# Kernel optimization log

Hardware: AMD Instinct MI355X
Metric: run time of the kernel (lower is better)

## Reference

```python
import jax, jax.numpy as jnp
import numpy as np

N = 50000   # nodes
E = 409600  # edges
H = 2       # heads
C = 64      # per-head channels


def _seg_softmax(alpha, dst, n):
    # PyG-style softmax over edges grouped by destination node. alpha: [E, H]
    m = jax.ops.segment_max(alpha, dst, num_segments=n)
    m = jnp.where(jnp.isfinite(m), m, 0.0)
    ex = jnp.exp(alpha - m[dst])
    s = jax.ops.segment_sum(ex, dst, num_segments=n)
    return ex / (s[dst] + 1e-16)


def _tconv(x, src, dst, e, Wq, bq, Wk, bk, Wv, bv, We, Ws, bs, n):
    # PyG TransformerConv (concat=True, beta=False, root_weight=True, dropout=0)
    q = (x @ Wq + bq).reshape(n, H, C)
    k = (x @ Wk + bk).reshape(n, H, C)
    v = (x @ Wv + bv).reshape(n, H, C)
    eh = (e @ We).reshape(-1, H, C)          # lin_edge has no bias in PyG
    kj = k[src] + eh                          # [E, H, C]
    alpha = (q[dst] * kj).sum(-1) / jnp.sqrt(jnp.float32(C))  # [E, H]
    alpha = _seg_softmax(alpha, dst, n)
    msg = (v[src] + eh) * alpha[:, :, None]   # [E, H, C]
    out = jax.ops.segment_sum(msg, dst, num_segments=n).reshape(n, H * C)
    return out + x @ Ws + bs                  # root/skip connection


def setup_inputs() -> dict:
    key = jax.random.key(0)
    ks = jax.random.split(key, 32)

    def lin_w(k, i, o):
        return (jax.random.normal(k, (i, o), dtype=jnp.float32) / np.sqrt(i)).astype(jnp.float32)

    inp = {
        "x": jax.random.normal(ks[0], (N, 6), dtype=jnp.float32),
        "edge_index": jax.random.randint(ks[1], (2, E), 0, N, dtype=jnp.int32).astype(jnp.int64),
        "edge_attr": jax.random.normal(ks[2], (E, 1), dtype=jnp.float32),
        # edge encoder: Linear(1, 64)
        "We_enc": lin_w(ks[3], 1, 64), "be_enc": jnp.zeros((64,), jnp.float32),
        # conv1: TransformerConv(6, 64, heads=2, edge_dim=64)
        "Wq1": lin_w(ks[4], 6, H * C), "bq1": jnp.zeros((H * C,), jnp.float32),
        "Wk1": lin_w(ks[5], 6, H * C), "bk1": jnp.zeros((H * C,), jnp.float32),
        "Wv1": lin_w(ks[6], 6, H * C), "bv1": jnp.zeros((H * C,), jnp.float32),
        "We1": lin_w(ks[7], 64, H * C),
        "Ws1": lin_w(ks[8], 6, H * C), "bs1": jnp.zeros((H * C,), jnp.float32),
        # conv2: TransformerConv(128, 64, heads=2, edge_dim=64)
        "Wq2": lin_w(ks[9], 128, H * C), "bq2": jnp.zeros((H * C,), jnp.float32),
        "Wk2": lin_w(ks[10], 128, H * C), "bk2": jnp.zeros((H * C,), jnp.float32),
        "Wv2": lin_w(ks[11], 128, H * C), "bv2": jnp.zeros((H * C,), jnp.float32),
        "We2": lin_w(ks[12], 64, H * C),
        "Ws2": lin_w(ks[13], 128, H * C), "bs2": jnp.zeros((H * C,), jnp.float32),
        # fc: Linear(128, 1)
        "Wfc": lin_w(ks[14], 128, 1), "bfc": jnp.zeros((1,), jnp.float32),
    }
    return inp


def reference(x, edge_index, edge_attr,
              We_enc, be_enc,
              Wq1, bq1, Wk1, bk1, Wv1, bv1, We1, Ws1, bs1,
              Wq2, bq2, Wk2, bk2, Wv2, bv2, We2, Ws2, bs2,
              Wfc, bfc):
    src, dst = edge_index[0], edge_index[1]
    e = edge_attr @ We_enc + be_enc           # [E, 64]
    h = jax.nn.relu(_tconv(x, src, dst, e, Wq1, bq1, Wk1, bk1, Wv1, bv1, We1, Ws1, bs1, N))
    h = jax.nn.relu(_tconv(h, src, dst, e, Wq2, bq2, Wk2, bk2, Wv2, bv2, We2, Ws2, bs2, N))
    return h @ Wfc + bfc                      # [N, 1]
```

## Files before the change

kernel.cpp:

```cpp
#include <hip/hip_runtime.h>


#define HC 128

typedef __attribute__((ext_vector_type(8))) short bf16x8;
typedef __attribute__((ext_vector_type(4))) float f32x4;

__device__ __forceinline__ unsigned bf16_rne(float f) {
    unsigned u = __float_as_uint(f);
    return (u + 0x7fffu + ((u >> 16) & 1u)) >> 16;
}

__global__ void k_uc(const float* __restrict__ We_enc, const float* __restrict__ be_enc,
                     const float* __restrict__ We1, const float* __restrict__ We2,
                     float* __restrict__ uc) {
    int c = threadIdx.x;
    float u1 = 0.f, c1 = 0.f, u2 = 0.f, c2 = 0.f;
    for (int j = 0; j < 64; ++j) {
        float we = We_enc[j], be = be_enc[j];
        float w1 = We1[j * HC + c], w2 = We2[j * HC + c];
        u1 += we * w1; c1 += be * w1;
        u2 += we * w2; c2 += be * w2;
    }
    uc[c] = u1; uc[HC + c] = c1; uc[2 * HC + c] = u2; uc[3 * HC + c] = c2;
}

__global__ __launch_bounds__(256) void k_wpack(
    const float* __restrict__ Wq, const float* __restrict__ Wk,
    const float* __restrict__ Wv, const float* __restrict__ Ws,
    unsigned short* __restrict__ Bph) {
    int t = blockIdx.x * 256 + threadIdx.x;
    int nn = t >> 7;
    int kk = t & 127;
    int mat = nn >> 7, c = nn & 127;
    const float* W = (mat == 0) ? Wq : (mat == 1) ? Wk : (mat == 2) ? Wv : Ws;
    Bph[nn * 128 + kk] = (unsigned short)bf16_rne(W[kk * 128 + c]);
}

__global__ __launch_bounds__(256) void k_hist(const int* __restrict__ ei, int* __restrict__ deg, int E) {
    int t = blockIdx.x * blockDim.x + threadIdx.x;
    if (t < E) atomicAdd(&deg[ei[E + t]], 1);
}

__global__ __launch_bounds__(256) void k_scan1(const int* __restrict__ deg, int* __restrict__ bsum, int n) {
    int t = blockIdx.x * 256 + threadIdx.x;
    int v = (t < n) ? deg[t] : 0;
#pragma unroll
    for (int off = 1; off < 64; off <<= 1) v += __shfl_xor(v, off);
    __shared__ int wsum[4];
    int lane = threadIdx.x & 63, w = threadIdx.x >> 6;
    if (lane == 0) wsum[w] = v;
    __syncthreads();
    if (threadIdx.x == 0) bsum[blockIdx.x] = wsum[0] + wsum[1] + wsum[2] + wsum[3];
}

__global__ __launch_bounds__(256) void k_scan2(int* __restrict__ bsum, int nb) {
    __shared__ int sh[256];
    int t = threadIdx.x;
    int v = (t < nb) ? bsum[t] : 0;
    sh[t] = v;
    __syncthreads();
    for (int off = 1; off < 256; off <<= 1) {
        int x = (t >= off) ? sh[t - off] : 0;
        __syncthreads();
        sh[t] += x;
        __syncthreads();
    }
    if (t < nb) bsum[t] = sh[t] - v;
}

__global__ __launch_bounds__(256) void k_scan3(const int* __restrict__ deg, const int* __restrict__ bsum,
                                               int* __restrict__ rowptr, int n, int E) {
    int t = blockIdx.x * 256 + threadIdx.x;
    int tid = threadIdx.x;
    int v = (t < n) ? deg[t] : 0;
    __shared__ int sh[256];
    sh[tid] = v;
    __syncthreads();
    for (int off = 1; off < 256; off <<= 1) {
        int x = (tid >= off) ? sh[tid - off] : 0;
        __syncthreads();
        sh[tid] += x;
        __syncthreads();
    }
    if (t < n) rowptr[t] = bsum[blockIdx.x] + sh[tid] - v;
    if (t == 0) rowptr[n] = E;
}

__global__ __launch_bounds__(256) void k_scatter(const int* __restrict__ ei, const int* __restrict__ rowptr,
                                                 int* __restrict__ cursor, int* __restrict__ eid, int E) {
    int t = blockIdx.x * blockDim.x + threadIdx.x;
    if (t >= E) return;
    int dst = ei[E + t];
    int pos = rowptr[dst] + atomicAdd(&cursor[dst], 1);
    eid[pos] = t;
}

__global__ __launch_bounds__(256) void k_bsort(const int* __restrict__ rowptr, int* __restrict__ eid, int n) {
    int t = blockIdx.x * blockDim.x + threadIdx.x;
    if (t >= n) return;
    int b = rowptr[t], e = rowptr[t + 1];
    for (int i = b + 1; i < e; ++i) {
        int key = eid[i];
        int j = i - 1;
        while (j >= b && eid[j] > key) { eid[j + 1] = eid[j]; --j; }
        eid[j + 1] = key;
    }
}

__global__ __launch_bounds__(256) void k_gather(const int* __restrict__ eid, const int* __restrict__ ei,
                                                const float* __restrict__ ea,
                                                int* __restrict__ srcs, float* __restrict__ eas, int E) {
    int t = blockIdx.x * blockDim.x + threadIdx.x;
    if (t >= E) return;
    int id = eid[t];
    srcs[t] = ei[id];
    eas[t] = ea[id];
}

__global__ __launch_bounds__(256) void k_lin6(
    const float* __restrict__ X, int n,
    const float* __restrict__ Wq, const float* __restrict__ bq,
    const float* __restrict__ Wk, const float* __restrict__ bk,
    const float* __restrict__ Wv, const float* __restrict__ bv,
    const float* __restrict__ Ws, const float* __restrict__ bs,
    float* __restrict__ q, unsigned short* __restrict__ kv,
    float* __restrict__ o) {
    __shared__ float xs[16][6];
    const int base = blockIdx.x * 16;
    const int tid = threadIdx.x;
    for (int i = tid; i < 16 * 6; i += 256) {
        int ni = base + i / 6;
        xs[i / 6][i % 6] = (ni < n) ? X[(size_t)ni * 6 + (i % 6)] : 0.f;
    }
    __syncthreads();
    const int c = tid & 127;
    const int m = tid >> 7;
    const float* WA = m ? Wv : Wq;
    const float* WB = m ? Ws : Wk;
    float accA[16], accB[16];
#pragma unroll
    for (int i = 0; i < 16; ++i) { accA[i] = 0.f; accB[i] = 0.f; }
    for (int j = 0; j < 6; ++j) {
        float w0 = WA[j * HC + c];
        float w1 = WB[j * HC + c];
#pragma unroll
        for (int i = 0; i < 16; ++i) {
            float xv = xs[i][j];
            accA[i] += xv * w0;
            accB[i] += xv * w1;
        }
    }
    if (m == 0) {
        const float bA = bq[c], bB = bk[c];
#pragma unroll
        for (int i = 0; i < 16; ++i) {
            int ni = base + i;
            if (ni < n) {
                q[(size_t)ni * HC + c] = accA[i] + bA;
                kv[(size_t)ni * 256 + c] = (unsigned short)bf16_rne(accB[i] + bB);
            }
        }
    } else {
        const float bA = bv[c], bB = bs[c];
#pragma unroll
        for (int i = 0; i < 16; ++i) {
            int ni = base + i;
            if (ni < n) {
                kv[(size_t)ni * 256 + 128 + c] = (unsigned short)bf16_rne(accA[i] + bA);
                o[(size_t)ni * HC + c] = accB[i] + bB;
            }
        }
    }
}

__global__ __launch_bounds__(256, 4) void k_lin2(
    const unsigned short* __restrict__ hb, const unsigned short* __restrict__ Bph,
    const float* __restrict__ bq, const float* __restrict__ bk,
    const float* __restrict__ bv, const float* __restrict__ bs,
    float* __restrict__ q, unsigned short* __restrict__ kv,
    float* __restrict__ o, int n) {
    __shared__ unsigned short Bs[128][128];
    const int tid = threadIdx.x;
    const int wid = tid >> 6, l = tid & 63;
    const int la = l & 15, lk = l >> 4;
    const int mb = blockIdx.x * 64;
    int nodeA = mb + wid * 16 + la;
    if (nodeA >= n) nodeA = n - 1;
    const int sw = (la & 7) << 3;
    const int crow0 = mb + wid * 16 + lk * 4;

    bf16x8 areg[4];
#pragma unroll
    for (int ks = 0; ks < 4; ++ks)
        areg[ks] = *(const bf16x8*)&hb[(size_t)nodeA * 128 + lk * 8 + ks * 32];

    for (int cq = 0; cq < 4; ++cq) {
        if (cq) __syncthreads();
        for (int i = tid; i < 128 * 16; i += 256) {
            int kk8 = i & 15;
            int nnl = i >> 4;
            bf16x8 val = *(const bf16x8*)&Bph[((size_t)(cq * 128 + nnl)) * 128 + kk8 * 8];
            int swk = (kk8 ^ (nnl & 7)) * 8;
            *(bf16x8*)&Bs[nnl][swk] = val;
        }
        __syncthreads();

        f32x4 acc[8];
#pragma unroll
        for (int nt = 0; nt < 8; ++nt) acc[nt] = (f32x4){0.f, 0.f, 0.f, 0.f};
#pragma unroll
        for (int ks = 0; ks < 4; ++ks) {
            const int rk = (lk * 8 + ks * 32) ^ sw;
#pragma unroll
            for (int nt = 0; nt < 8; ++nt) {
                bf16x8 Bh = *(const bf16x8*)&Bs[nt * 16 + la][rk];
                acc[nt] = __builtin_amdgcn_mfma_f32_16x16x32_bf16(areg[ks], Bh, acc[nt], 0, 0, 0);
            }
        }
        const float* bias = (cq == 0) ? bq : (cq == 1) ? bk : (cq == 2) ? bv : bs;
#pragma unroll
        for (int nt = 0; nt < 8; ++nt) {
            const int col = nt * 16 + la;
            const float bb = bias[col];
            if (cq == 0 || cq == 3) {
                float* out = (cq == 0) ? q : o;
#pragma unroll
                for (int j = 0; j < 4; ++j) {
                    int n0 = crow0 + j;
                    if (n0 < n) out[(size_t)n0 * 128 + col] = acc[nt][j] + bb;
                }
            } else {
                const int co = (cq == 1) ? col : 128 + col;
#pragma unroll
                for (int j = 0; j < 4; ++j) {
                    int n0 = crow0 + j;
                    if (n0 < n) kv[(size_t)n0 * 256 + co] = (unsigned short)bf16_rne(acc[nt][j] + bb);
                }
            }
        }
    }
}

template <int MODE>
__global__ __launch_bounds__(256) void k_attn(
    const float* __restrict__ q, const unsigned short* __restrict__ kvp,
    const int* __restrict__ rowptr, const int* __restrict__ srcs, const float* __restrict__ eas,
    const float* __restrict__ ucu, const float* __restrict__ ucc,
    float* __restrict__ io, unsigned short* __restrict__ hb, int n) {
    int wid = (int)((blockIdx.x * (size_t)blockDim.x + threadIdx.x) >> 6);
    int lane = threadIdx.x & 63;
    if (wid >= n) return;
    const int half = lane >> 5;
    const int hl = lane & 31;
    const int ch = hl * 4;

    float4 qr = *(const float4*)&q[(size_t)wid * 128 + ch];
    float4 uu = *(const float4*)&ucu[ch];
    float4 cc = *(const float4*)&ucc[ch];

    float qu = qr.x * uu.x + qr.y * uu.y + qr.z * uu.z + qr.w * uu.w;
    float qc = qr.x * cc.x + qr.y * cc.y + qr.z * cc.z + qr.w * cc.w;
#pragma unroll
    for (int off = 1; off < 16; off <<= 1) {
        qu += __shfl_xor(qu, off);
        qc += __shfl_xor(qc, off);
    }

    int b = rowptr[wid], e = rowptr[wid + 1];
    float m = -3.0e38f, s = 0.f, sea = 0.f;
    float av0 = 0.f, av1 = 0.f, av2 = 0.f, av3 = 0.f;

    if (b < e) {
        int pi = b + half;
        bool val = pi < e;
        int pc = val ? pi : e - 1;
        int src = srcs[pc];
        float eav = eas[pc];
        const unsigned short* row = &kvp[(size_t)src * 256 + ch];
        uint2 ku = *(const uint2*)row;
        uint2 vu = *(const uint2*)(row + 128);
        for (int p = b; p < e; p += 2) {
            int pn = p + 2 + half;
            bool valn = pn < e;
            int pcn = valn ? pn : e - 1;
            int srcn = srcs[pcn];
            float eavn = eas[pcn];
            const unsigned short* rown = &kvp[(size_t)srcn * 256 + ch];
            uint2 kun = *(const uint2*)rown;
            uint2 vun = *(const uint2*)(rown + 128);

            float k0 = __uint_as_float(ku.x << 16);
            float k1 = __uint_as_float(ku.x & 0xffff0000u);
            float k2 = __uint_as_float(ku.y << 16);
            float k3 = __uint_as_float(ku.y & 0xffff0000u);
            float d = qr.x * k0 + qr.y * k1 + qr.z * k2 + qr.w * k3;
#pragma unroll
            for (int off = 1; off < 16; off <<= 1) d += __shfl_xor(d, off);
            float a = val ? (d + fmaf(eav, qu, qc)) * 0.125f : -INFINITY;
            float nm = fmaxf(m, a);
            float sc = __expf(m - nm);
            float pw = __expf(a - nm);
            float v0 = __uint_as_float(vu.x << 16);
            float v1 = __uint_as_float(vu.x & 0xffff0000u);
            float v2 = __uint_as_float(vu.y << 16);
            float v3 = __uint_as_float(vu.y & 0xffff0000u);
            s = fmaf(s, sc, pw);
            sea = fmaf(sea, sc, pw * eav);
            av0 = fmaf(av0, sc, pw * v0);
            av1 = fmaf(av1, sc, pw * v1);
            av2 = fmaf(av2, sc, pw * v2);
            av3 = fmaf(av3, sc, pw * v3);
            m = nm;
            ku = kun; vu = vun; eav = eavn; val = valn;
        }
    }

    {
        float om = __shfl_xor(m, 32);
        float os = __shfl_xor(s, 32);
        float osea = __shfl_xor(sea, 32);
        float o0 = __shfl_xor(av0, 32);
        float o1 = __shfl_xor(av1, 32);
        float o2 = __shfl_xor(av2, 32);
        float o3 = __shfl_xor(av3, 32);
        float nm = fmaxf(m, om);
        float scS = __expf(m - nm);
        float scO = __expf(om - nm);
        s = s * scS + os * scO;
        sea = sea * scS + osea * scO;
        av0 = av0 * scS + o0 * scO;
        av1 = av1 * scS + o1 * scO;
        av2 = av2 * scS + o2 * scO;
        av3 = av3 * scS + o3 * scO;
    }

    if (half == 0) {
        float inv = 1.f / (s + 1e-16f);
        float4 skip = *(const float4*)&io[(size_t)wid * 128 + ch];
        float r0 = (av0 + uu.x * sea + cc.x * s) * inv + skip.x;
        float r1 = (av1 + uu.y * sea + cc.y * s) * inv + skip.y;
        float r2 = (av2 + uu.z * sea + cc.z * s) * inv + skip.z;
        float r3 = (av3 + uu.w * sea + cc.w * s) * inv + skip.w;
        if (MODE == 1) {
            r0 = fmaxf(r0, 0.f); r1 = fmaxf(r1, 0.f);
            r2 = fmaxf(r2, 0.f); r3 = fmaxf(r3, 0.f);
            ushort4 hv = make_ushort4((unsigned short)bf16_rne(r0),
                                      (unsigned short)bf16_rne(r1),
                                      (unsigned short)bf16_rne(r2),
                                      (unsigned short)bf16_rne(r3));
            *(ushort4*)&hb[(size_t)wid * 128 + ch] = hv;
        } else {
            *(float4*)&io[(size_t)wid * 128 + ch] = make_float4(r0, r1, r2, r3);
        }
    }
}

__global__ __launch_bounds__(256) void k_fc(
    const float* __restrict__ h, const float* __restrict__ Wfc,
    const float* __restrict__ bfc, float* __restrict__ out, int n) {
    int w = (int)((blockIdx.x * (size_t)blockDim.x + threadIdx.x) >> 6);
    int lane = threadIdx.x & 63;
    if (w >= n) return;
    const float2* h2 = (const float2*)h;
    const float2* w2 = (const float2*)Wfc;
    float2 hv = h2[(size_t)w * 64 + lane];
    float2 wv = w2[lane];
    float vsum = fmaxf(hv.x, 0.f) * wv.x + fmaxf(hv.y, 0.f) * wv.y;
#pragma unroll
    for (int off = 1; off < 64; off <<= 1) vsum += __shfl_xor(vsum, off);
    if (lane == 0) out[w] = vsum + bfc[0];
}

extern "C" void kernel_launch(void* const* d_in, const int* in_sizes, int n_in,
                              void* d_out, int out_size, void* d_ws, size_t ws_size,
                              hipStream_t stream) {
    const float* x      = (const float*)d_in[0];
    const int*   ei     = (const int*)d_in[1];
    const float* ea     = (const float*)d_in[2];
    const float* We_enc = (const float*)d_in[3];
    const float* be_enc = (const float*)d_in[4];
    const float* Wq1 = (const float*)d_in[5],  *bq1 = (const float*)d_in[6];
    const float* Wk1 = (const float*)d_in[7],  *bk1 = (const float*)d_in[8];
    const float* Wv1 = (const float*)d_in[9],  *bv1 = (const float*)d_in[10];
    const float* We1 = (const float*)d_in[11];
    const float* Ws1 = (const float*)d_in[12], *bs1 = (const float*)d_in[13];
    const float* Wq2 = (const float*)d_in[14], *bq2 = (const float*)d_in[15];
    const float* Wk2 = (const float*)d_in[16], *bk2 = (const float*)d_in[17];
    const float* Wv2 = (const float*)d_in[18], *bv2 = (const float*)d_in[19];
    const float* We2 = (const float*)d_in[20];
    const float* Ws2 = (const float*)d_in[21], *bs2 = (const float*)d_in[22];
    const float* Wfc = (const float*)d_in[23], *bfc = (const float*)d_in[24];

    const int n = in_sizes[0] / 6;
    const int E = in_sizes[2];

    float* ws = (float*)d_ws;
    size_t off = 0;
    float* qb = ws + off; off += (size_t)n * HC;
    float* Bb = ws + off; off += (size_t)n * HC;
    unsigned short* kv16 = (unsigned short*)(ws + off); off += (size_t)n * HC;
    int* rowptr = (int*)(ws + off); off += (size_t)(n + 1);
    int* deg    = (int*)(ws + off); off += (size_t)n;
    int* bsum   = (int*)(ws + off); off += 256;
    int* eid    = (int*)(ws + off); off += (size_t)E;
    int* srcs   = (int*)(ws + off); off += (size_t)E;
    float* eas  = ws + off; off += (size_t)E;
    float* uc   = ws + off; off += 512;
    unsigned short* hb16 = (unsigned short*)(ws + off); off += (size_t)n * HC / 2;
    unsigned short* Bph = (unsigned short*)(ws + off); off += 512 * 128 / 2;

    const int eb = (E + 255) / 256;
    const int nb = (n + 255) / 256;
    const int wb = (int)(((size_t)n * 64 + 255) / 256);

    hipLaunchKernelGGL(k_uc, dim3(1), dim3(128), 0, stream, We_enc, be_enc, We1, We2, uc);
    hipLaunchKernelGGL(k_wpack, dim3(256), dim3(256), 0, stream, Wq2, Wk2, Wv2, Ws2, Bph);

    hipMemsetAsync(deg, 0, (size_t)n * sizeof(int), stream);
    hipLaunchKernelGGL(k_hist, dim3(eb), dim3(256), 0, stream, ei, deg, E);
    hipLaunchKernelGGL(k_scan1, dim3(nb), dim3(256), 0, stream, deg, bsum, n);
    hipLaunchKernelGGL(k_scan2, dim3(1), dim3(256), 0, stream, bsum, nb);
    hipLaunchKernelGGL(k_scan3, dim3(nb), dim3(256), 0, stream, deg, bsum, rowptr, n, E);
    hipMemsetAsync(deg, 0, (size_t)n * sizeof(int), stream);
    hipLaunchKernelGGL(k_scatter, dim3(eb), dim3(256), 0, stream, ei, rowptr, deg, eid, E);
    hipLaunchKernelGGL(k_bsort, dim3(nb), dim3(256), 0, stream, rowptr, eid, n);
    hipLaunchKernelGGL(k_gather, dim3(eb), dim3(256), 0, stream, eid, ei, ea, srcs, eas, E);

    hipLaunchKernelGGL(k_lin6, dim3((n + 15) / 16), dim3(256), 0, stream,
                       x, n, Wq1, bq1, Wk1, bk1, Wv1, bv1, Ws1, bs1, qb, kv16, Bb);
    hipLaunchKernelGGL((k_attn<1>), dim3(wb), dim3(256), 0, stream,
                       qb, kv16, rowptr, srcs, eas, uc, uc + HC, Bb, hb16, n);

    hipLaunchKernelGGL(k_lin2, dim3((n + 63) / 64), dim3(256), 0, stream,
                       hb16, Bph, bq2, bk2, bv2, bs2, qb, kv16, Bb, n);
    hipLaunchKernelGGL((k_attn<0>), dim3(wb), dim3(256), 0, stream,
                       qb, kv16, rowptr, srcs, eas, uc + 2 * HC, uc + 3 * HC, Bb,
                       (unsigned short*)nullptr, n);

    hipLaunchKernelGGL(k_fc, dim3(wb), dim3(256), 0, stream, Bb, Wfc, bfc, (float*)d_out, n);
}
```

Before: 231.7 us.

## Fuse gather into sort, fc into attention, store q in bf16, widen attention lanes

Several changes land together. The edge gather is merged into the per-node insertion sort, and the degree reset moves into the scan kernel so one memset disappears. The final fc layer is fused into the second attention kernel's epilogue. The query vectors are stored as bf16, and the attention kernel now processes four edges at a time per wave, with 8 channels per lane and bf16 dot2 instructions. The goal is fewer launches and less memory traffic, at the cost of extra bf16 rounding on q and a serialized gather inside the sort threads.

```diff
diff --git a/kernel.cpp b/kernel.cpp
--- a/kernel.cpp
+++ b/kernel.cpp
@@ -5,11 +5,19 @@
 
 typedef __attribute__((ext_vector_type(8))) short bf16x8;
 typedef __attribute__((ext_vector_type(4))) float f32x4;
+#if __has_builtin(__builtin_amdgcn_fdot2_f32_bf16)
+typedef __attribute__((ext_vector_type(2))) __bf16 bf16x2;
+#define HAS_DOT2 1
+#else
+#define HAS_DOT2 0
+#endif
 
 __device__ __forceinline__ unsigned bf16_rne(float f) {
     unsigned u = __float_as_uint(f);
     return (u + 0x7fffu + ((u >> 16) & 1u)) >> 16;
 }
+__device__ __forceinline__ float blo(unsigned u) { return __uint_as_float(u << 16); }
+__device__ __forceinline__ float bhi(unsigned u) { return __uint_as_float(u & 0xffff0000u); }
 
 __global__ void k_uc(const float* __restrict__ We_enc, const float* __restrict__ be_enc,
                      const float* __restrict__ We1, const float* __restrict__ We2,
@@ -69,7 +77,7 @@
     if (t < nb) bsum[t] = sh[t] - v;
 }
 
-__global__ __launch_bounds__(256) void k_scan3(const int* __restrict__ deg, const int* __restrict__ bsum,
+__global__ __launch_bounds__(256) void k_scan3(int* __restrict__ deg, const int* __restrict__ bsum,
                                                int* __restrict__ rowptr, int n, int E) {
     int t = blockIdx.x * 256 + threadIdx.x;
     int tid = threadIdx.x;
@@ -83,7 +91,7 @@
         sh[tid] += x;
         __syncthreads();
     }
-    if (t < n) rowptr[t] = bsum[blockIdx.x] + sh[tid] - v;
+    if (t < n) { rowptr[t] = bsum[blockIdx.x] + sh[tid] - v; deg[t] = 0; }
     if (t == 0) rowptr[n] = E;
 }
 
@@ -96,7 +104,10 @@
     eid[pos] = t;
 }
 
-__global__ __launch_bounds__(256) void k_bsort(const int* __restrict__ rowptr, int* __restrict__ eid, int n) {
+__global__ __launch_bounds__(256) void k_bsortg(
+    const int* __restrict__ rowptr, int* __restrict__ eid,
+    const int* __restrict__ ei, const float* __restrict__ ea,
+    int* __restrict__ srcs, float* __restrict__ eas, int n) {
     int t = blockIdx.x * blockDim.x + threadIdx.x;
     if (t >= n) return;
     int b = rowptr[t], e = rowptr[t + 1];
@@ -106,16 +117,11 @@
         while (j >= b && eid[j] > key) { eid[j + 1] = eid[j]; --j; }
         eid[j + 1] = key;
     }
-}
-
-__global__ __launch_bounds__(256) void k_gather(const int* __restrict__ eid, const int* __restrict__ ei,
-                                                const float* __restrict__ ea,
-                                                int* __restrict__ srcs, float* __restrict__ eas, int E) {
-    int t = blockIdx.x * blockDim.x + threadIdx.x;
-    if (t >= E) return;
-    int id = eid[t];
-    srcs[t] = ei[id];
-    eas[t] = ea[id];
+    for (int i = b; i < e; ++i) {
+        int id = eid[i];
+        srcs[i] = ei[id];
+        eas[i] = ea[id];
+    }
 }
 
 __global__ __launch_bounds__(256) void k_lin6(
@@ -124,7 +130,7 @@
     const float* __restrict__ Wk, const float* __restrict__ bk,
     const float* __restrict__ Wv, const float* __restrict__ bv,
     const float* __restrict__ Ws, const float* __restrict__ bs,
-    float* __restrict__ q, unsigned short* __restrict__ kv,
+    unsigned short* __restrict__ q16, unsigned short* __restrict__ kv,
     float* __restrict__ o) {
     __shared__ float xs[16][6];
     const int base = blockIdx.x * 16;
@@ -157,7 +163,7 @@
         for (int i = 0; i < 16; ++i) {
             int ni = base + i;
             if (ni < n) {
-                q[(size_t)ni * HC + c] = accA[i] + bA;
+                q16[(size_t)ni * HC + c] = (unsigned short)bf16_rne(accA[i] + bA);
                 kv[(size_t)ni * 256 + c] = (unsigned short)bf16_rne(accB[i] + bB);
             }
         }
@@ -178,7 +184,7 @@
     const unsigned short* __restrict__ hb, const unsigned short* __restrict__ Bph,
     const float* __restrict__ bq, const float* __restrict__ bk,
     const float* __restrict__ bv, const float* __restrict__ bs,
-    float* __restrict__ q, unsigned short* __restrict__ kv,
+    unsigned short* __restrict__ q16, unsigned short* __restrict__ kv,
     float* __restrict__ o, int n) {
     __shared__ unsigned short Bs[128][128];
     const int tid = threadIdx.x;
@@ -223,12 +229,17 @@
         for (int nt = 0; nt < 8; ++nt) {
             const int col = nt * 16 + la;
             const float bb = bias[col];
-            if (cq == 0 || cq == 3) {
-                float* out = (cq == 0) ? q : o;
+            if (cq == 3) {
 #pragma unroll
                 for (int j = 0; j < 4; ++j) {
                     int n0 = crow0 + j;
-                    if (n0 < n) out[(size_t)n0 * 128 + col] = acc[nt][j] + bb;
+                    if (n0 < n) o[(size_t)n0 * 128 + col] = acc[nt][j] + bb;
+                }
+            } else if (cq == 0) {
+#pragma unroll
+                for (int j = 0; j < 4; ++j) {
+                    int n0 = crow0 + j;
+                    if (n0 < n) q16[(size_t)n0 * 128 + col] = (unsigned short)bf16_rne(acc[nt][j] + bb);
                 }
             } else {
                 const int co = (cq == 1) ? col : 128 + col;
@@ -244,25 +255,34 @@
 
 template <int MODE>
 __global__ __launch_bounds__(256) void k_attn(
-    const float* __restrict__ q, const unsigned short* __restrict__ kvp,
+    const unsigned short* __restrict__ q16, const unsigned short* __restrict__ kvp,
     const int* __restrict__ rowptr, const int* __restrict__ srcs, const float* __restrict__ eas,
     const float* __restrict__ ucu, const float* __restrict__ ucc,
-    float* __restrict__ io, unsigned short* __restrict__ hb, int n) {
+    const float* __restrict__ io, unsigned short* __restrict__ hb,
+    const float* __restrict__ Wfc, const float* __restrict__ bfc,
+    float* __restrict__ out, int n) {
     int wid = (int)((blockIdx.x * (size_t)blockDim.x + threadIdx.x) >> 6);
     int lane = threadIdx.x & 63;
     if (wid >= n) return;
     const int half = lane >> 5;
-    const int hl = lane & 31;
-    const int ch = hl * 4;
-
-    float4 qr = *(const float4*)&q[(size_t)wid * 128 + ch];
-    float4 uu = *(const float4*)&ucu[ch];
-    float4 cc = *(const float4*)&ucc[ch];
-
-    float qu = qr.x * uu.x + qr.y * uu.y + qr.z * uu.z + qr.w * uu.w;
-    float qc = qr.x * cc.x + qr.y * cc.y + qr.z * cc.z + qr.w * cc.w;
-#pragma unroll
-    for (int off = 1; off < 16; off <<= 1) {
+    const int sub = (lane >> 4) & 1;
+    const int grp = lane >> 4;
+    const int hl = lane & 15;
+    const int ch = hl * 8;
+    const int strm = half + 2 * sub;
+
+    uint4 qp = *(const uint4*)&q16[(size_t)wid * 128 + ch];
+    float qf0 = blo(qp.x), qf1 = bhi(qp.x), qf2 = blo(qp.y), qf3 = bhi(qp.y);
+    float qf4 = blo(qp.z), qf5 = bhi(qp.z), qf6 = blo(qp.w), qf7 = bhi(qp.w);
+    float4 uuA = *(const float4*)&ucu[ch], uuB = *(const float4*)&ucu[ch + 4];
+    float4 ccA = *(const float4*)&ucc[ch], ccB = *(const float4*)&ucc[ch + 4];
+
+    float qu = qf0 * uuA.x + qf1 * uuA.y + qf2 * uuA.z + qf3 * uuA.w
+             + qf4 * uuB.x + qf5 * uuB.y + qf6 * uuB.z + qf7 * uuB.w;
+    float qc = qf0 * ccA.x + qf1 * ccA.y + qf2 * ccA.z + qf3 * ccA.w
+             + qf4 * ccB.x + qf5 * ccB.y + qf6 * ccB.z + qf7 * ccB.w;
+#pragma unroll
+    for (int off = 1; off < 8; off <<= 1) {
         qu += __shfl_xor(qu, off);
         qc += __shfl_xor(qc, off);
     }
@@ -270,106 +290,113 @@
     int b = rowptr[wid], e = rowptr[wid + 1];
     float m = -3.0e38f, s = 0.f, sea = 0.f;
     float av0 = 0.f, av1 = 0.f, av2 = 0.f, av3 = 0.f;
+    float av4 = 0.f, av5 = 0.f, av6 = 0.f, av7 = 0.f;
 
     if (b < e) {
-        int pi = b + half;
+        int pi = b + strm;
         bool val = pi < e;
         int pc = val ? pi : e - 1;
         int src = srcs[pc];
         float eav = eas[pc];
         const unsigned short* row = &kvp[(size_t)src * 256 + ch];
-        uint2 ku = *(const uint2*)row;
-        uint2 vu = *(const uint2*)(row + 128);
-        for (int p = b; p < e; p += 2) {
-            int pn = p + 2 + half;
+        uint4 ku = *(const uint4*)row;
+        uint4 vu = *(const uint4*)(row + 128);
+        for (int p = b; p < e; p += 4) {
+            int pn = p + 4 + strm;
             bool valn = pn < e;
             int pcn = valn ? pn : e - 1;
             int srcn = srcs[pcn];
             float eavn = eas[pcn];
             const unsigned short* rown = &kvp[(size_t)srcn * 256 + ch];
-            uint2 kun = *(const uint2*)rown;
-            uint2 vun = *(const uint2*)(rown + 128);
-
-            float k0 = __uint_as_float(ku.x << 16);
-            float k1 = __uint_as_float(ku.x & 0xffff0000u);
-            float k2 = __uint_as_float(ku.y << 16);
-            float k3 = __uint_as_float(ku.y & 0xffff0000u);
-            float d = qr.x * k0 + qr.y * k1 + qr.z * k2 + qr.w * k3;
-#pragma unroll
-            for (int off = 1; off < 16; off <<= 1) d += __shfl_xor(d, off);
+            uint4 kun = *(const uint4*)rown;
+            uint4 vun = *(const uint4*)(rown + 128);
+
+            float d;
+#if HAS_DOT2
+            d = __builtin_amdgcn_fdot2_f32_bf16(
+                    __builtin_bit_cast(bf16x2, ku.x), __builtin_bit_cast(bf16x2, qp.x),
+                __builtin_amdgcn_fdot2_f32_bf16(
+                    __builtin_bit_cast(bf16x2, ku.y), __builtin_bit_cast(bf16x2, qp.y),
+                __builtin_amdgcn_fdot2_f32_bf16(
+                    __builtin_bit_cast(bf16x2, ku.z), __builtin_bit_cast(bf16x2, qp.z),
+                __builtin_amdgcn_fdot2_f32_bf16(
+                    __builtin_bit_cast(bf16x2, ku.w), __builtin_bit_cast(bf16x2, qp.w),
+                    0.f, false), false), false), false);
+#else
+            d = qf0 * blo(ku.x) + qf1 * bhi(ku.x) + qf2 * blo(ku.y) + qf3 * bhi(ku.y)
+              + qf4 * blo(ku.z) + qf5 * bhi(ku.z) + qf6 * blo(ku.w) + qf7 * bhi(ku.w);
+#endif
+            d += __shfl_xor(d, 1); d += __shfl_xor(d, 2); d += __shfl_xor(d, 4);
             float a = val ? (d + fmaf(eav, qu, qc)) * 0.125f : -INFINITY;
             float nm = fmaxf(m, a);
             float sc = __expf(m - nm);
             float pw = __expf(a - nm);
-            float v0 = __uint_as_float(vu.x << 16);
-            float v1 = __uint_as_float(vu.x & 0xffff0000u);
-            float v2 = __uint_as_float(vu.y << 16);
-            float v3 = __uint_as_float(vu.y & 0xffff0000u);
             s = fmaf(s, sc, pw);
             sea = fmaf(sea, sc, pw * eav);
-            av0 = fmaf(av0, sc, pw * v0);
-            av1 = fmaf(av1, sc, pw * v1);
-            av2 = fmaf(av2, sc, pw * v2);
-            av3 = fmaf(av3, sc, pw * v3);
+            av0 = fmaf(av0, sc, pw * blo(vu.x));
+            av1 = fmaf(av1, sc, pw * bhi(vu.x));
+            av2 = fmaf(av2, sc, pw * blo(vu.y));
+            av3 = fmaf(av3, sc, pw * bhi(vu.y));
+            av4 = fmaf(av4, sc, pw * blo(vu.z));
+            av5 = fmaf(av5, sc, pw * bhi(vu.z));
+            av6 = fmaf(av6, sc, pw * blo(vu.w));
+            av7 = fmaf(av7, sc, pw * bhi(vu.w));
             m = nm;
             ku = kun; vu = vun; eav = eavn; val = valn;
         }
     }
 
-    {
-        float om = __shfl_xor(m, 32);
-        float os = __shfl_xor(s, 32);
-        float osea = __shfl_xor(sea, 32);
-        float o0 = __shfl_xor(av0, 32);
-        float o1 = __shfl_xor(av1, 32);
-        float o2 = __shfl_xor(av2, 32);
-        float o3 = __shfl_xor(av3, 32);
+#pragma unroll
+    for (int M = 16; M <= 32; M <<= 1) {
+        float om = __shfl_xor(m, M);
+        float os = __shfl_xor(s, M);
+        float osea = __shfl_xor(sea, M);
+        float o0 = __shfl_xor(av0, M), o1 = __shfl_xor(av1, M);
+        float o2 = __shfl_xor(av2, M), o3 = __shfl_xor(av3, M);
+        float o4 = __shfl_xor(av4, M), o5 = __shfl_xor(av5, M);
+        float o6 = __shfl_xor(av6, M), o7 = __shfl_xor(av7, M);
         float nm = fmaxf(m, om);
         float scS = __expf(m - nm);
         float scO = __expf(om - nm);
         s = s * scS + os * scO;
         sea = sea * scS + osea * scO;
-        av0 = av0 * scS + o0 * scO;
-        av1 = av1 * scS + o1 * scO;
-        av2 = av2 * scS + o2 * scO;
-        av3 = av3 * scS + o3 * scO;
-    }
-
-    if (half == 0) {
-        float inv = 1.f / (s + 1e-16f);
-        float4 skip = *(const float4*)&io[(size_t)wid * 128 + ch];
-        float r0 = (av0 + uu.x * sea + cc.x * s) * inv + skip.x;
-        float r1 = (av1 + uu.y * sea + cc.y * s) * inv + skip.y;
-        float r2 = (av2 + uu.z * sea + cc.z * s) * inv + skip.z;
-        float r3 = (av3 + uu.w * sea + cc.w * s) * inv + skip.w;
-        if (MODE == 1) {
-            r0 = fmaxf(r0, 0.f); r1 = fmaxf(r1, 0.f);
-            r2 = fmaxf(r2, 0.f); r3 = fmaxf(r3, 0.f);
-            ushort4 hv = make_ushort4((unsigned short)bf16_rne(r0),
-                                      (unsigned short)bf16_rne(r1),
-                                      (unsigned short)bf16_rne(r2),
-                                      (unsigned short)bf16_rne(r3));
-            *(ushort4*)&hb[(size_t)wid * 128 + ch] = hv;
-        } else {
-            *(float4*)&io[(size_t)wid * 128 + ch] = make_float4(r0, r1, r2, r3);
-        }
-    }
-}
-
-__global__ __launch_bounds__(256) void k_fc(
-    const float* __restrict__ h, const float* __restrict__ Wfc,
-    const float* __restrict__ bfc, float* __restrict__ out, int n) {
-    int w = (int)((blockIdx.x * (size_t)blockDim.x + threadIdx.x) >> 6);
-    int lane = threadIdx.x & 63;
-    if (w >= n) return;
-    const float2* h2 = (const float2*)h;
-    const float2* w2 = (const float2*)Wfc;
-    float2 hv = h2[(size_t)w * 64 + lane];
-    float2 wv = w2[lane];
-    float vsum = fmaxf(hv.x, 0.f) * wv.x + fmaxf(hv.y, 0.f) * wv.y;
-#pragma unroll
-    for (int off = 1; off < 64; off <<= 1) vsum += __shfl_xor(vsum, off);
-    if (lane == 0) out[w] = vsum + bfc[0];
+        av0 = av0 * scS + o0 * scO; av1 = av1 * scS + o1 * scO;
+        av2 = av2 * scS + o2 * scO; av3 = av3 * scS + o3 * scO;
+        av4 = av4 * scS + o4 * scO; av5 = av5 * scS + o5 * scO;
+        av6 = av6 * scS + o6 * scO; av7 = av7 * scS + o7 * scO;
+        m = nm;
+    }
+
+    float inv = 1.f / (s + 1e-16f);
+    float4 skA = *(const float4*)&io[(size_t)wid * 128 + ch];
+    float4 skB = *(const float4*)&io[(size_t)wid * 128 + ch + 4];
+    float r0 = fmaxf((av0 + uuA.x * sea + ccA.x * s) * inv + skA.x, 0.f);
+    float r1 = fmaxf((av1 + uuA.y * sea + ccA.y * s) * inv + skA.y, 0.f);
+    float r2 = fmaxf((av2 + uuA.z * sea + ccA.z * s) * inv + skA.z, 0.f);
+    float r3 = fmaxf((av3 + uuA.w * sea + ccA.w * s) * inv + skA.w, 0.f);
+    float r4 = fmaxf((av4 + uuB.x * sea + ccB.x * s) * inv + skB.x, 0.f);
+    float r5 = fmaxf((av5 + uuB.y * sea + ccB.y * s) * inv + skB.y, 0.f);
+    float r6 = fmaxf((av6 + uuB.z * sea + ccB.z * s) * inv + skB.z, 0.f);
+    float r7 = fmaxf((av7 + uuB.w * sea + ccB.w * s) * inv + skB.w, 0.f);
+
+    if (MODE == 1) {
+        if (grp == 0) {
+            uint4 hv;
+            hv.x = bf16_rne(r0) | (bf16_rne(r1) << 16);
+            hv.y = bf16_rne(r2) | (bf16_rne(r3) << 16);
+            hv.z = bf16_rne(r4) | (bf16_rne(r5) << 16);
+            hv.w = bf16_rne(r6) | (bf16_rne(r7) << 16);
+            *(uint4*)&hb[(size_t)wid * 128 + ch] = hv;
+        }
+    } else {
+        float4 wfA = *(const float4*)&Wfc[ch];
+        float4 wfB = *(const float4*)&Wfc[ch + 4];
+        float rr = r0 * wfA.x + r1 * wfA.y + r2 * wfA.z + r3 * wfA.w
+                 + r4 * wfB.x + r5 * wfB.y + r6 * wfB.z + r7 * wfB.w;
+#pragma unroll
+        for (int off = 1; off < 16; off <<= 1) rr += __shfl_xor(rr, off);
+        if (lane == 0) out[wid] = rr + bfc[0];
+    }
 }
 
 extern "C" void kernel_launch(void* const* d_in, const int* in_sizes, int n_in,
@@ -397,7 +424,7 @@
 
     float* ws = (float*)d_ws;
     size_t off = 0;
-    float* qb = ws + off; off += (size_t)n * HC;
+    unsigned short* qb16 = (unsigned short*)(ws + off); off += (size_t)n * HC / 2;
     float* Bb = ws + off; off += (size_t)n * HC;
     unsigned short* kv16 = (unsigned short*)(ws + off); off += (size_t)n * HC;
     int* rowptr = (int*)(ws + off); off += (size_t)(n + 1);
@@ -422,21 +449,18 @@
     hipLaunchKernelGGL(k_scan1, dim3(nb), dim3(256), 0, stream, deg, bsum, n);
     hipLaunchKernelGGL(k_scan2, dim3(1), dim3(256), 0, stream, bsum, nb);
     hipLaunchKernelGGL(k_scan3, dim3(nb), dim3(256), 0, stream, deg, bsum, rowptr, n, E);
-    hipMemsetAsync(deg, 0, (size_t)n * sizeof(int), stream);
     hipLaunchKernelGGL(k_scatter, dim3(eb), dim3(256), 0, stream, ei, rowptr, deg, eid, E);
-    hipLaunchKernelGGL(k_bsort, dim3(nb), dim3(256), 0, stream, rowptr, eid, n);
-    hipLaunchKernelGGL(k_gather, dim3(eb), dim3(256), 0, stream, eid, ei, ea, srcs, eas, E);
+    hipLaunchKernelGGL(k_bsortg, dim3(nb), dim3(256), 0, stream, rowptr, eid, ei, ea, srcs, eas, n);
 
     hipLaunchKernelGGL(k_lin6, dim3((n + 15) / 16), dim3(256), 0, stream,
-                       x, n, Wq1, bq1, Wk1, bk1, Wv1, bv1, Ws1, bs1, qb, kv16, Bb);
+                       x, n, Wq1, bq1, Wk1, bk1, Wv1, bv1, Ws1, bs1, qb16, kv16, Bb);
     hipLaunchKernelGGL((k_attn<1>), dim3(wb), dim3(256), 0, stream,
-                       qb, kv16, rowptr, srcs, eas, uc, uc + HC, Bb, hb16, n);
+                       qb16, kv16, rowptr, srcs, eas, uc, uc + HC, Bb, hb16,
+                       Wfc, bfc, (float*)d_out, n);
 
     hipLaunchKernelGGL(k_lin2, dim3((n + 63) / 64), dim3(256), 0, stream,
-                       hb16, Bph, bq2, bk2, bv2, bs2, qb, kv16, Bb, n);
+                       hb16, Bph, bq2, bk2, bv2, bs2, qb16, kv16, Bb, n);
     hipLaunchKernelGGL((k_attn<0>), dim3(wb), dim3(256), 0, stream,
-                       qb, kv16, rowptr, srcs, eas, uc + 2 * HC, uc + 3 * HC, Bb,
-                       (unsigned short*)nullptr, n);
-
-    hipLaunchKernelGGL(k_fc, dim3(wb), dim3(256), 0, stream, Bb, Wfc, bfc, (float*)d_out, n);
-}
+                       qb16, kv16, rowptr, srcs, eas, uc + 2 * HC, uc + 3 * HC, Bb,
+                       (unsigned short*)nullptr, Wfc, bfc, (float*)d_out, n);
+}
```

New measurement: 218.5 us. -5.7%, faster.
